# Optimization experiments

Measured on AMD Instinct MI355X. Metric: run time of the kernel, lower is better.

Reference implementation:

```python
import jax, jax.numpy as jnp
import numpy as np

NUM_HEADS = 16

def _apply_rope(x, cos, sin):
    # x: (B, H, T, D); cos/sin: (T, D//2)
    B, H, T, D = x.shape
    xr = x.reshape(B, H, T, D // 2, 2)
    x0, x1 = xr[..., 0], xr[..., 1]
    c = cos[None, None, :, :]
    s = sin[None, None, :, :]
    out = jnp.stack([x0 * c - x1 * s, x0 * s + x1 * c], axis=-1)
    return out.reshape(B, H, T, D)


def setup_inputs() -> dict:
    key = jax.random.key(0)
    k1, k2, k3 = jax.random.split(key, 3)
    B, T, C = 2, 2048, 1024
    D = C // NUM_HEADS
    x = jax.random.normal(k1, (B, T, C), dtype=jnp.float32)
    qkv_w = jax.random.normal(k2, (3 * C, C), dtype=jnp.float32) * (C ** -0.5)
    proj_w = jax.random.normal(k3, (C, C), dtype=jnp.float32) * (C ** -0.5)
    # standard RoPE frequency table (theta = 10000)
    inv_freq = 1.0 / (10000.0 ** (jnp.arange(0, D, 2, dtype=jnp.float32) / D))  # (D/2,)
    angles = jnp.arange(T, dtype=jnp.float32)[:, None] * inv_freq[None, :]      # (T, D/2)
    return {
        "x": x,
        "freqs_cos": jnp.cos(angles),
        "freqs_sin": jnp.sin(angles),
        "qkv_w": qkv_w,
        "proj_w": proj_w,
    }


def reference(x, freqs_cos, freqs_sin, qkv_w, proj_w):
    B, T, C = x.shape
    H = NUM_HEADS
    D = C // H
    qkv = x @ qkv_w.T                                  # (B, T, 3C)
    q, k, v = jnp.split(qkv, 3, axis=-1)
    q = q.reshape(B, T, H, D).transpose(0, 2, 1, 3)    # (B, H, T, D)
    k = k.reshape(B, T, H, D).transpose(0, 2, 1, 3)
    v = v.reshape(B, T, H, D).transpose(0, 2, 1, 3)
    q = _apply_rope(q, freqs_cos, freqs_sin)
    k = _apply_rope(k, freqs_cos, freqs_sin)
    scale = 1.0 / jnp.sqrt(jnp.asarray(D, dtype=x.dtype))
    scores = jnp.einsum('bhqd,bhkd->bhqk', q, k) * scale
    causal = jnp.tril(jnp.ones((T, T), dtype=bool))
    scores = jnp.where(causal[None, None], scores, jnp.finfo(scores.dtype).min)
    attn = jax.nn.softmax(scores, axis=-1)
    out = jnp.einsum('bhqk,bhkd->bhqd', attn, v)       # (B, H, T, D)
    out = out.transpose(0, 2, 1, 3).reshape(B, T, C)
    return out @ proj_w.T
```

## Files before the change

### kernel.cpp

```cpp
#include <hip/hip_runtime.h>
#include <stdint.h>

#define DI __device__ __forceinline__

typedef unsigned short u16;
typedef __bf16 bf16x8 __attribute__((ext_vector_type(8)));
typedef unsigned short u16x8 __attribute__((ext_vector_type(8)));
typedef unsigned short u16x4 __attribute__((ext_vector_type(4)));
typedef float f32x4 __attribute__((ext_vector_type(4)));
typedef float f32x16 __attribute__((ext_vector_type(16)));
typedef unsigned int u32x2 __attribute__((ext_vector_type(2)));
typedef unsigned int u32x4 __attribute__((ext_vector_type(4)));

DI u16 f2bf(float f) { __bf16 h = (__bf16)f; return __builtin_bit_cast(u16, h); }
DI float bf2f(u16 u) { return (float)__builtin_bit_cast(__bf16, u); }

DI bf16x8 ld8(const u16* p) { return __builtin_bit_cast(bf16x8, *(const u16x8*)p); }

DI f32x4 mfma16(bf16x8 a, bf16x8 b, f32x4 c) {
  return __builtin_amdgcn_mfma_f32_16x16x32_bf16(a, b, c, 0, 0, 0);
}
DI f32x16 mfma32(bf16x8 a, bf16x8 b, f32x16 c) {
  return __builtin_amdgcn_mfma_f32_32x32x16_bf16(a, b, c, 0, 0, 0);
}

DI unsigned pkbf(float a, float b) {
  unsigned r;
  asm("v_cvt_pk_bf16_f32 %0, %1, %2" : "=v"(r) : "v"(a), "v"(b));
  return r;
}

DI void async16(const u16* g, u16* l) {
  __builtin_amdgcn_global_load_lds((const __attribute__((address_space(1))) void*)g,
                                   (__attribute__((address_space(3))) void*)l, 16, 0, 0);
}

__global__ __launch_bounds__(256) void cast_all(const float* __restrict__ x,
                                                const float* __restrict__ qw,
                                                const float* __restrict__ pw,
                                                u16* __restrict__ xb, u16* __restrict__ qwb,
                                                u16* __restrict__ pwb) {
  const int bi = blockIdx.x;
  const float* src;
  u16* dst;
  int off;
  if (bi < 4096) {
    src = x; dst = xb; off = bi;
  } else if (bi < 7168) {
    src = qw; dst = qwb; off = bi - 4096;
  } else {
    src = pw; dst = pwb; off = bi - 7168;
  }
  const int i = off * 256 + threadIdx.x;
  const float4 v = ((const float4*)src)[i];
  u16x4 o = {f2bf(v.x), f2bf(v.y), f2bf(v.z), f2bf(v.w)};
  ((u16x4*)dst)[i] = o;
}

template <int OUT_BF16>
__global__ __launch_bounds__(256) void gemm_bt(const u16* __restrict__ A,
                                               const u16* __restrict__ W,
                                               void* __restrict__ outp,
                                               int M, int N, int K) {
  __shared__ u16 sA[2 * 4096];
  __shared__ u16 sB[2 * 4096];
  const int tid = threadIdx.x;
  const int w = tid >> 6, L = tid & 63;
  const int lo = L & 15, quad = L >> 4;
  const int nb = N >> 7;
  const int bm = blockIdx.x / nb, bn = blockIdx.x - bm * nb;
  const int m0 = bm << 7, n0 = bn << 7;
  const int wm = (w >> 1) << 6, wn = (w & 1) << 6;

  f32x4 acc[4][4];
#pragma unroll
  for (int i = 0; i < 4; ++i)
#pragma unroll
    for (int j = 0; j < 4; ++j) acc[i][j] = 0.f;

  const int r0 = tid >> 2, s0 = tid & 3;
  const int c0 = s0 ^ ((r0 >> 1) & 3);
  const int r1 = r0 + 64;
  const int c1 = s0 ^ ((r1 >> 1) & 3);
  const u16* aP0 = A + (size_t)(m0 + r0) * K + c0 * 8;
  const u16* aP1 = A + (size_t)(m0 + r1) * K + c1 * 8;
  const u16* bP0 = W + (size_t)(n0 + r0) * K + c0 * 8;
  const u16* bP1 = W + (size_t)(n0 + r1) * K + c1 * 8;
  u16* ldA0 = &sA[tid * 8];
  u16* ldA1 = &sA[(tid + 256) * 8];
  u16* ldB0 = &sB[tid * 8];
  u16* ldB1 = &sB[(tid + 256) * 8];

  int raf[4], rbf[4];
#pragma unroll
  for (int mt = 0; mt < 4; ++mt) {
    int r = wm + mt * 16 + lo;
    raf[mt] = r * 32 + ((quad ^ ((r >> 1) & 3)) << 3);
    r = wn + mt * 16 + lo;
    rbf[mt] = r * 32 + ((quad ^ ((r >> 1) & 3)) << 3);
  }

  auto stage = [&](int buf) {
    const int bo = buf << 12;
    async16(aP0, ldA0 + bo);
    async16(aP1, ldA1 + bo);
    async16(bP0, ldB0 + bo);
    async16(bP1, ldB1 + bo);
    aP0 += 32; aP1 += 32; bP0 += 32; bP1 += 32;
  };

  const int kIters = K >> 5;
  stage(0);
  for (int kt = 0; kt < kIters; ++kt) {
    __syncthreads();
    if (kt + 1 < kIters) stage((kt + 1) & 1);
    const int bo = (kt & 1) << 12;
    bf16x8 af[4], bfr[4];
#pragma unroll
    for (int mt = 0; mt < 4; ++mt) af[mt] = ld8(&sA[bo + raf[mt]]);
#pragma unroll
    for (int nt = 0; nt < 4; ++nt) bfr[nt] = ld8(&sB[bo + rbf[nt]]);
#pragma unroll
    for (int mt = 0; mt < 4; ++mt)
#pragma unroll
      for (int nt = 0; nt < 4; ++nt)
        acc[mt][nt] = mfma16(af[mt], bfr[nt], acc[mt][nt]);
  }

#pragma unroll
  for (int mt = 0; mt < 4; ++mt) {
    const int m = m0 + wm + mt * 16 + quad * 4;
#pragma unroll
    for (int nt = 0; nt < 4; ++nt) {
      const int n = n0 + wn + nt * 16 + lo;
#pragma unroll
      for (int r = 0; r < 4; ++r) {
        const size_t off = (size_t)(m + r) * N + n;
        if (OUT_BF16)
          ((u16*)outp)[off] = f2bf(acc[mt][nt][r]);
        else
          ((float*)outp)[off] = acc[mt][nt][r];
      }
    }
  }
}

#define QSCALE 0.18033688011112f
__global__ __launch_bounds__(256) void ropevt_k(const u16* __restrict__ qkv,
                                                const float* __restrict__ cosb,
                                                const float* __restrict__ sinb,
                                                u16* __restrict__ qo, u16* __restrict__ ko,
                                                u16* __restrict__ vto) {
  __shared__ u16 sT[64 * 64];
  const int tid = threadIdx.x;
  if (blockIdx.x < 8192) {
    const int idx = blockIdx.x * 256 + tid;
    const int i = idx & 31;
    const int t = (idx >> 5) & 2047;
    const int h = (idx >> 16) & 15;
    const int b = idx >> 20;
    const size_t src = ((size_t)(b * 2048 + t)) * 3072 + h * 64 + 2 * i;
    const float q0v = bf2f(qkv[src]), q1v = bf2f(qkv[src + 1]);
    const float k0v = bf2f(qkv[src + 1024]), k1v = bf2f(qkv[src + 1025]);
    const float c = cosb[t * 32 + i], s = sinb[t * 32 + i];
    const size_t dst = ((size_t)((b * 16 + h) * 2048 + t)) * 64 + 2 * i;
    qo[dst] = f2bf((q0v * c - q1v * s) * QSCALE);
    qo[dst + 1] = f2bf((q0v * s + q1v * c) * QSCALE);
    ko[dst] = f2bf(k0v * c - k1v * s);
    ko[dst + 1] = f2bf(k0v * s + k1v * c);
  } else {
    const int bi = blockIdx.x - 8192;
    const int bh = bi & 31;
    const int t0 = (bi >> 5) << 6;
    const int b = bh >> 4, h = bh & 15;
#pragma unroll
    for (int it = 0; it < 2; ++it) {
      const int id = tid + it * 256;
      const int tr = id >> 3, s = id & 7, c = s ^ (tr & 7);
      async16(qkv + (size_t)(b * 2048 + t0 + tr) * 3072 + 2048 + h * 64 + c * 8, &sT[id * 8]);
    }
    __syncthreads();
#pragma unroll
    for (int it = 0; it < 2; ++it) {
      const int id = tid + it * 256;
      const int d = id >> 3, ct = id & 7;
      u16x8 o;
#pragma unroll
      for (int j = 0; j < 8; ++j) {
        const int t = ct * 8 + j;
        o[j] = sT[t * 64 + (((d >> 3) ^ (t & 7)) << 3) + (d & 7)];
      }
      *(u16x8*)(vto + ((size_t)bh * 64 + d) * 2048 + t0 + ct * 8) = o;
    }
  }
}

__global__ __launch_bounds__(256, 2) void fattn_part(const u16* __restrict__ qs,
                                                     const u16* __restrict__ ks,
                                                     const u16* __restrict__ vtb,
                                                     u16* __restrict__ opart,
                                                     float* __restrict__ lbuf) {
  __shared__ u16 sK[2 * 4096];
  __shared__ u16 sVt[2 * 4096];
  const int tid = threadIdx.x;
  const int w = tid >> 6, L = tid & 63;
  const int col = L & 31, hi = L >> 5;
  const int raw = blockIdx.x;
  const int part = raw & 1;
  const int bh = (raw >> 1) & 31;
  const int qb = 15 - (raw >> 6);
  const int n = 2 * qb + 2;
  const int h0 = qb + 1;
  const int tk0 = part ? h0 : 0;
  const int tk1 = part ? n : h0;
  const size_t hoff = (size_t)bh * (2048 * 64);
  const int q0 = qb << 7;
  const int wq = q0 + w * 32;

  const int kvA = tid >> 3, cA = (tid & 7) ^ (kvA & 7);
  const int idB = tid + 256;
  const int kvB = idB >> 3, cB = (idB & 7) ^ (kvB & 7);
  const u16* kP0 = ks + hoff + (size_t)(tk0 * 64 + kvA) * 64 + cA * 8;
  const u16* kP1 = ks + hoff + (size_t)(tk0 * 64 + kvB) * 64 + cB * 8;
  const u16* vP0 = vtb + hoff + (size_t)kvA * 2048 + tk0 * 64 + cA * 8;
  const u16* vP1 = vtb + hoff + (size_t)kvB * 2048 + tk0 * 64 + cB * 8;
  u16* ldK0 = &sK[tid * 8];
  u16* ldK1 = &sK[idB * 8];
  u16* ldV0 = &sVt[tid * 8];
  u16* ldV1 = &sVt[idB * 8];

  auto stage = [&](int buf) {
    const int bo = buf << 12;
    async16(kP0, ldK0 + bo);
    async16(kP1, ldK1 + bo);
    async16(vP0, ldV0 + bo);
    async16(vP1, ldV1 + bo);
    kP0 += 4096; kP1 += 4096; vP0 += 64; vP1 += 64;
  };

  int kaOff[2][4];
#pragma unroll
  for (int mt = 0; mt < 2; ++mt) {
    const int row = mt * 32 + col;
#pragma unroll
    for (int ksI = 0; ksI < 4; ++ksI)
      kaOff[mt][ksI] = row * 64 + (((ksI * 2 + hi) ^ (row & 7)) << 3);
  }

  bf16x8 qf[4];
#pragma unroll
  for (int ksI = 0; ksI < 4; ++ksI)
    qf[ksI] = ld8(qs + hoff + (size_t)(wq + col) * 64 + ksI * 16 + hi * 8);

  bf16x8 ones;
#pragma unroll
  for (int j = 0; j < 8; ++j) ones[j] = (__bf16)1.0f;

  f32x16 lacc = 0.f;
  f32x16 ot0 = 0.f, ot1 = 0.f;

  const int ntk = tk1 - tk0;
  stage(0);
  for (int it2 = 0; it2 < ntk; ++it2) {
    __syncthreads();
    if (it2 + 1 < ntk) stage((it2 + 1) & 1);
    const int bo = (it2 & 1) << 12;
    const int kt = tk0 + it2;

    if (64 * kt <= wq + 31) {
      f32x16 st0 = 0.f, st1 = 0.f;
#pragma unroll
      for (int ksI = 0; ksI < 4; ++ksI) {
        st0 = mfma32(ld8(&sK[bo + kaOff[0][ksI]]), qf[ksI], st0);
        st1 = mfma32(ld8(&sK[bo + kaOff[1][ksI]]), qf[ksI], st1);
      }
      if (64 * kt + 63 > wq) {
        const int qg = wq + col;
        const int kvb = 64 * kt + 4 * hi;
#pragma unroll
        for (int r = 0; r < 16; ++r) {
          const int kvr = kvb + (r & 3) + 8 * (r >> 2);
          if (kvr > qg) st0[r] = -3.0e38f;
          if (kvr + 32 > qg) st1[r] = -3.0e38f;
        }
      }
      bf16x8 pf[4];
#pragma unroll
      for (int mt = 0; mt < 2; ++mt) {
        const f32x16 sv = mt ? st1 : st0;
        f32x16 p;
#pragma unroll
        for (int r = 0; r < 16; ++r) p[r] = __builtin_amdgcn_exp2f(sv[r]);
        {
          unsigned x0 = pkbf(p[0], p[1]), x1 = pkbf(p[2], p[3]);
          unsigned y0 = pkbf(p[4], p[5]), y1 = pkbf(p[6], p[7]);
          u32x2 r02 = __builtin_amdgcn_permlane32_swap(x0, y0, false, false);
          u32x2 r13 = __builtin_amdgcn_permlane32_swap(x1, y1, false, false);
          u32x4 wv = {r02[0], r13[0], r02[1], r13[1]};
          pf[2 * mt] = __builtin_bit_cast(bf16x8, wv);
        }
        {
          unsigned x0 = pkbf(p[8], p[9]), x1 = pkbf(p[10], p[11]);
          unsigned y0 = pkbf(p[12], p[13]), y1 = pkbf(p[14], p[15]);
          u32x2 r02 = __builtin_amdgcn_permlane32_swap(x0, y0, false, false);
          u32x2 r13 = __builtin_amdgcn_permlane32_swap(x1, y1, false, false);
          u32x4 wv = {r02[0], r13[0], r02[1], r13[1]};
          pf[2 * mt + 1] = __builtin_bit_cast(bf16x8, wv);
        }
      }
#pragma unroll
      for (int ksI = 0; ksI < 4; ++ksI) lacc = mfma32(ones, pf[ksI], lacc);
#pragma unroll
      for (int ksI = 0; ksI < 4; ++ksI) {
        ot0 = mfma32(ld8(&sVt[bo + kaOff[0][ksI]]), pf[ksI], ot0);
        ot1 = mfma32(ld8(&sVt[bo + kaOff[1][ksI]]), pf[ksI], ot1);
      }
    }
  }

  const int q = wq + col;
  const int pq = bh * 32 + (q >> 6);
  u16* ob = opart + (size_t)(part * 1024 + pq) * 4096 + (size_t)(q & 63) * 64;
#pragma unroll
  for (int mtd = 0; mtd < 2; ++mtd) {
    const f32x16 o = mtd ? ot1 : ot0;
#pragma unroll
    for (int rg = 0; rg < 4; ++rg) {
      const int d0 = mtd * 32 + rg * 8 + hi * 4;
      u16x4 ok = {f2bf(o[rg * 4 + 0]), f2bf(o[rg * 4 + 1]),
                  f2bf(o[rg * 4 + 2]), f2bf(o[rg * 4 + 3])};
      *(u16x4*)&ob[d0] = ok;
    }
  }
  if (hi == 0) lbuf[(size_t)(part * 1024 + pq) * 64 + (q & 63)] = lacc[0];
}

__global__ __launch_bounds__(256) void fattn_merge(const u16* __restrict__ opart,
                                                   const float* __restrict__ lbuf,
                                                   u16* __restrict__ aout) {
  const int pq = blockIdx.x;
  const int bh = pq >> 5, qi = pq & 31;
  const int b = bh >> 4, h = bh & 15;
  const int tid = threadIdx.x;
#pragma unroll
  for (int it = 0; it < 2; ++it) {
    const int idx = tid + it * 256;
    const int q = idx >> 3, d0 = (idx & 7) * 8;
    const float l0 = lbuf[(size_t)pq * 64 + q];
    const float l1 = lbuf[(size_t)(1024 + pq) * 64 + q];
    const float inv = 1.f / (l0 + l1);
    const u16x8 o0 = *(const u16x8*)&opart[(size_t)pq * 4096 + q * 64 + d0];
    const u16x8 o1 = *(const u16x8*)&opart[(size_t)(1024 + pq) * 4096 + q * 64 + d0];
    u16x8 o;
#pragma unroll
    for (int j = 0; j < 8; ++j) o[j] = f2bf((bf2f(o0[j]) + bf2f(o1[j])) * inv);
    *(u16x8*)&aout[((size_t)(b * 2048 + qi * 64 + q)) * 1024 + h * 64 + d0] = o;
  }
}

extern "C" void kernel_launch(void* const* d_in, const int* in_sizes, int n_in,
                              void* d_out, int out_size, void* d_ws, size_t ws_size,
                              hipStream_t stream) {
  const float* x = (const float*)d_in[0];
  const float* fcos = (const float*)d_in[1];
  const float* fsin = (const float*)d_in[2];
  const float* qkvw = (const float*)d_in[3];
  const float* projw = (const float*)d_in[4];
  float* out = (float*)d_out;

  char* ws = (char*)d_ws;
  u16* x_bf = (u16*)(ws);
  u16* qkvw_bf = (u16*)(ws + (8u << 20));
  u16* projw_bf = (u16*)(ws + (14u << 20));
  u16* qkv_bf = (u16*)(ws + (16u << 20));
  u16* q_bf = (u16*)(ws + (40u << 20));
  u16* k_bf = (u16*)(ws + (48u << 20));
  u16* vt = (u16*)(ws + (56u << 20));
  u16* attn_bf = (u16*)(ws + (64u << 20));
  u16* opart = (u16*)(ws + (16u << 20));
  float* lbuf = (float*)(ws + (32u << 20));

  cast_all<<<8192, 256, 0, stream>>>(x, qkvw, projw, x_bf, qkvw_bf, projw_bf);
  gemm_bt<1><<<768, 256, 0, stream>>>(x_bf, qkvw_bf, (void*)qkv_bf, 4096, 3072, 1024);
  ropevt_k<<<9216, 256, 0, stream>>>(qkv_bf, fcos, fsin, q_bf, k_bf, vt);
  fattn_part<<<1024, 256, 0, stream>>>(q_bf, k_bf, vt, opart, lbuf);
  fattn_merge<<<1024, 256, 0, stream>>>(opart, lbuf, attn_bf);
  gemm_bt<0><<<256, 256, 0, stream>>>(attn_bf, projw_bf, (void*)out, 4096, 1024, 1024);
}
```

Baseline: 186.3 us.

## Add 256x256 pipelined QKV GEMM, vectorize RoPE, prioritize attention MFMAs

Replaces the QKV projection GEMM with a new 512-thread kernel that computes 256x256 tiles. It uses a swizzled double-buffered LDS pipeline, fine-grained barriers, s_setprio around MFMA bursts and an XCD-aware block remap. The RoPE kernel now handles 8 elements per thread with 16-byte vector loads and stores instead of scalar accesses, cutting its grid from 9216 to 3072 blocks. The attention kernel wraps its MFMA sections in s_setprio to favor matrix issue across waves. Risks include LDS pressure limiting occupancy and only 192 workgroups for the QKV GEMM, which may leave some CUs underused.

Result: faster. 181.8 us (-2.4%).

```diff
diff --git a/kernel.cpp b/kernel.cpp
--- a/kernel.cpp
+++ b/kernel.cpp
@@ -33,6 +33,12 @@
 DI void async16(const u16* g, u16* l) {
   __builtin_amdgcn_global_load_lds((const __attribute__((address_space(1))) void*)g,
                                    (__attribute__((address_space(3))) void*)l, 16, 0, 0);
+}
+
+DI void barC() {
+  asm volatile("" ::: "memory");
+  __builtin_amdgcn_s_barrier();
+  asm volatile("" ::: "memory");
 }
 
 __global__ __launch_bounds__(256) void cast_all(const float* __restrict__ x,
@@ -57,6 +63,109 @@
   ((u16x4*)dst)[i] = o;
 }
 
+__global__ __launch_bounds__(512, 2) void gemm256(const u16* __restrict__ A,
+                                                  const u16* __restrict__ W,
+                                                  u16* __restrict__ outp,
+                                                  int M, int N, int K) {
+  __shared__ u16 sAB[65536];
+  const int tid = threadIdx.x;
+  const int w = tid >> 6, L = tid & 63;
+  const int lo = L & 15, quad = L >> 4;
+  const int wm128 = (w >> 2) * 128, wn64 = (w & 3) * 64;
+  const int nbn = N >> 8;
+  const int nwg = gridDim.x;
+  const int cpx = nwg >> 3;
+  const int raw = blockIdx.x;
+  const int bi = (raw & 7) * cpx + (raw >> 3);
+  const int bm = bi / nbn, bn = bi - bm * nbn;
+  const int m0 = bm << 8, n0 = bn << 8;
+  const int kSteps = K >> 6;
+
+  f32x4 acc[8][4];
+#pragma unroll
+  for (int i = 0; i < 8; ++i)
+#pragma unroll
+    for (int j = 0; j < 4; ++j) acc[i][j] = 0.f;
+
+  const int rS = tid >> 2;
+  const int scol = ((tid & 3) << 3) ^ ((tid & 32) ? 16 : 0);
+  const u16* Ap = A + (size_t)(m0 + rS) * K + scol;
+  const u16* Wp = W + (size_t)(n0 + rS) * K + scol;
+  auto STAGE = [&](int s, int mat, int kk) {
+    if (s >= kSteps) return;
+    const u16* g = (mat ? Wp : Ap) + s * 64 + kk * 32;
+    u16* l = sAB + ((s & 1) << 15) + (mat << 14) + (kk << 13) + tid * 8;
+    async16(g, l);
+    async16(g + (size_t)128 * K, l + 4096);
+  };
+
+  const int qoff = (quad << 3) ^ ((lo & 8) ? 16 : 0);
+  auto ldA = [&](int buf, int kk, int mh, int m2) {
+    const int R = wm128 + mh * 64 + m2 * 16 + lo;
+    return ld8(&sAB[(buf << 15) + (kk << 13) + R * 32 + qoff]);
+  };
+  auto ldB = [&](int buf, int kk, int nf) {
+    const int R = wn64 + nf * 16 + lo;
+    return ld8(&sAB[(buf << 15) + 16384 + (kk << 13) + R * 32 + qoff]);
+  };
+
+  bf16x8 bF[4];
+  auto PH = [&](int buf, int kk, int mh, bool loadB, int sS, int sM, int sK,
+                bool dovm, bool last) {
+    bf16x8 aF[4];
+#pragma unroll
+    for (int m2 = 0; m2 < 4; ++m2) aF[m2] = ldA(buf, kk, mh, m2);
+    if (loadB) {
+#pragma unroll
+      for (int nf = 0; nf < 4; ++nf) bF[nf] = ldB(buf, kk, nf);
+    }
+    STAGE(sS, sM, sK);
+    if (dovm) {
+      if (last)
+        asm volatile("s_waitcnt vmcnt(0)" ::: "memory");
+      else
+        asm volatile("s_waitcnt vmcnt(4)" ::: "memory");
+    }
+    barC();
+    __builtin_amdgcn_s_setprio(1);
+#pragma unroll
+    for (int m2 = 0; m2 < 4; ++m2)
+#pragma unroll
+      for (int nf = 0; nf < 4; ++nf)
+        acc[mh * 4 + m2][nf] = mfma16(aF[m2], bF[nf], acc[mh * 4 + m2][nf]);
+    __builtin_amdgcn_s_setprio(0);
+    barC();
+  };
+
+  STAGE(0, 0, 0); STAGE(0, 1, 0); STAGE(0, 0, 1); STAGE(0, 1, 1);
+  STAGE(1, 0, 0); STAGE(1, 1, 0);
+  asm volatile("s_waitcnt vmcnt(4)" ::: "memory");
+  barC();
+
+  for (int t = 0; t < kSteps; t += 2) {
+    const bool last = (t + 2) >= kSteps;
+    PH(0, 0, 0, true,  t + 1, 0, 1, false, last);
+    PH(0, 0, 1, false, t + 1, 1, 1, false, last);
+    PH(0, 1, 0, true,  t + 2, 0, 0, false, last);
+    PH(0, 1, 1, false, t + 2, 1, 0, true,  last);
+    PH(1, 0, 0, true,  t + 2, 0, 1, false, last);
+    PH(1, 0, 1, false, t + 2, 1, 1, false, last);
+    PH(1, 1, 0, true,  t + 3, 0, 0, false, last);
+    PH(1, 1, 1, false, t + 3, 1, 0, true,  last);
+  }
+
+#pragma unroll
+  for (int mf = 0; mf < 8; ++mf) {
+    const int m = m0 + wm128 + (mf >> 2) * 64 + (mf & 3) * 16 + quad * 4;
+#pragma unroll
+    for (int nf = 0; nf < 4; ++nf) {
+      const int nn = n0 + wn64 + nf * 16 + lo;
+#pragma unroll
+      for (int r = 0; r < 4; ++r) outp[(size_t)(m + r) * N + nn] = f2bf(acc[mf][nf][r]);
+    }
+  }
+}
+
 template <int OUT_BF16>
 __global__ __launch_bounds__(256) void gemm_bt(const u16* __restrict__ A,
                                                const u16* __restrict__ W,
@@ -153,23 +262,33 @@
                                                 u16* __restrict__ vto) {
   __shared__ u16 sT[64 * 64];
   const int tid = threadIdx.x;
-  if (blockIdx.x < 8192) {
+  if (blockIdx.x < 2048) {
     const int idx = blockIdx.x * 256 + tid;
-    const int i = idx & 31;
-    const int t = (idx >> 5) & 2047;
-    const int h = (idx >> 16) & 15;
-    const int b = idx >> 20;
-    const size_t src = ((size_t)(b * 2048 + t)) * 3072 + h * 64 + 2 * i;
-    const float q0v = bf2f(qkv[src]), q1v = bf2f(qkv[src + 1]);
-    const float k0v = bf2f(qkv[src + 1024]), k1v = bf2f(qkv[src + 1025]);
-    const float c = cosb[t * 32 + i], s = sinb[t * 32 + i];
-    const size_t dst = ((size_t)((b * 16 + h) * 2048 + t)) * 64 + 2 * i;
-    qo[dst] = f2bf((q0v * c - q1v * s) * QSCALE);
-    qo[dst + 1] = f2bf((q0v * s + q1v * c) * QSCALE);
-    ko[dst] = f2bf(k0v * c - k1v * s);
-    ko[dst + 1] = f2bf(k0v * s + k1v * c);
+    const int c = idx & 7;
+    const int h = (idx >> 3) & 15;
+    const int t = (idx >> 7) & 2047;
+    const int b = idx >> 18;
+    const size_t src = (size_t)(b * 2048 + t) * 3072 + h * 64 + c * 8;
+    const u16x8 qv = *(const u16x8*)&qkv[src];
+    const u16x8 kv = *(const u16x8*)&qkv[src + 1024];
+    const f32x4 cv = *(const f32x4*)&cosb[t * 32 + c * 4];
+    const f32x4 sv = *(const f32x4*)&sinb[t * 32 + c * 4];
+    u16x8 q8, k8;
+#pragma unroll
+    for (int j = 0; j < 4; ++j) {
+      const float cc = cv[j], ss = sv[j];
+      const float q0 = bf2f(qv[2 * j]), q1 = bf2f(qv[2 * j + 1]);
+      q8[2 * j] = f2bf((q0 * cc - q1 * ss) * QSCALE);
+      q8[2 * j + 1] = f2bf((q0 * ss + q1 * cc) * QSCALE);
+      const float k0 = bf2f(kv[2 * j]), k1 = bf2f(kv[2 * j + 1]);
+      k8[2 * j] = f2bf(k0 * cc - k1 * ss);
+      k8[2 * j + 1] = f2bf(k0 * ss + k1 * cc);
+    }
+    const size_t dst = (size_t)((b * 16 + h) * 2048 + t) * 64 + c * 8;
+    *(u16x8*)&qo[dst] = q8;
+    *(u16x8*)&ko[dst] = k8;
   } else {
-    const int bi = blockIdx.x - 8192;
+    const int bi = blockIdx.x - 2048;
     const int bh = bi & 31;
     const int t0 = (bi >> 5) << 6;
     const int b = bh >> 4, h = bh & 15;
@@ -269,11 +388,13 @@
 
     if (64 * kt <= wq + 31) {
       f32x16 st0 = 0.f, st1 = 0.f;
+      __builtin_amdgcn_s_setprio(1);
 #pragma unroll
       for (int ksI = 0; ksI < 4; ++ksI) {
         st0 = mfma32(ld8(&sK[bo + kaOff[0][ksI]]), qf[ksI], st0);
         st1 = mfma32(ld8(&sK[bo + kaOff[1][ksI]]), qf[ksI], st1);
       }
+      __builtin_amdgcn_s_setprio(0);
       if (64 * kt + 63 > wq) {
         const int qg = wq + col;
         const int kvb = 64 * kt + 4 * hi;
@@ -308,6 +429,7 @@
           pf[2 * mt + 1] = __builtin_bit_cast(bf16x8, wv);
         }
       }
+      __builtin_amdgcn_s_setprio(1);
 #pragma unroll
       for (int ksI = 0; ksI < 4; ++ksI) lacc = mfma32(ones, pf[ksI], lacc);
 #pragma unroll
@@ -315,6 +437,7 @@
         ot0 = mfma32(ld8(&sVt[bo + kaOff[0][ksI]]), pf[ksI], ot0);
         ot1 = mfma32(ld8(&sVt[bo + kaOff[1][ksI]]), pf[ksI], ot1);
       }
+      __builtin_amdgcn_s_setprio(0);
     }
   }
 
@@ -381,8 +504,8 @@
   float* lbuf = (float*)(ws + (32u << 20));
 
   cast_all<<<8192, 256, 0, stream>>>(x, qkvw, projw, x_bf, qkvw_bf, projw_bf);
-  gemm_bt<1><<<768, 256, 0, stream>>>(x_bf, qkvw_bf, (void*)qkv_bf, 4096, 3072, 1024);
-  ropevt_k<<<9216, 256, 0, stream>>>(qkv_bf, fcos, fsin, q_bf, k_bf, vt);
+  gemm256<<<192, 512, 0, stream>>>(x_bf, qkvw_bf, qkv_bf, 4096, 3072, 1024);
+  ropevt_k<<<3072, 256, 0, stream>>>(qkv_bf, fcos, fsin, q_bf, k_bf, vt);
   fattn_part<<<1024, 256, 0, stream>>>(q_bf, k_bf, vt, opart, lbuf);
   fattn_merge<<<1024, 256, 0, stream>>>(opart, lbuf, attn_bf);
   gemm_bt<0><<<256, 256, 0, stream>>>(attn_bf, projw_bf, (void*)out, 4096, 1024, 1024);
```
